# Kernel tuning notes

Measured on AMD Instinct MI355X. Metric: run time of the kernel, lower is better.

## Reference

```python
import jax, jax.numpy as jnp
import numpy as np

EMBED_DIM = 1024
NUM_HEADS = 16
HEAD_DIM = EMBED_DIM // NUM_HEADS


def setup_inputs() -> dict:
    key = jax.random.key(0)
    ks = jax.random.split(key, 9)
    B, T, C = 4, 2048, EMBED_DIM
    s = 1.0 / np.sqrt(C)
    return {
        "x": jax.random.normal(ks[0], (B, T, C), jnp.float32),
        "Wq": jax.random.normal(ks[1], (C, C), jnp.float32) * s,
        "bq": jnp.zeros((C,), jnp.float32),
        "Wk": jax.random.normal(ks[2], (C, C), jnp.float32) * s,
        "bk": jnp.zeros((C,), jnp.float32),
        "Wv": jax.random.normal(ks[3], (C, C), jnp.float32) * s,
        "bv": jnp.zeros((C,), jnp.float32),
        "Wo": jax.random.normal(ks[4], (C, C), jnp.float32) * s,
        "bo": jnp.zeros((C,), jnp.float32),
    }


def reference(x, Wq, bq, Wk, bk, Wv, bv, Wo, bo):
    B, T, C = x.shape
    H, D = NUM_HEADS, HEAD_DIM
    # projections (torch Linear: y = x @ W.T + b; here weights stored as [in, out])
    q = (x @ Wq + bq).reshape(B, T, H, D).transpose(0, 2, 1, 3)  # [B,H,T,D]
    k = (x @ Wk + bk).reshape(B, T, H, D).transpose(0, 2, 1, 3)
    v = (x @ Wv + bv).reshape(B, T, H, D).transpose(0, 2, 1, 3)
    scores = jnp.einsum("bhqd,bhkd->bhqk", q, k) / jnp.sqrt(jnp.float32(D))
    causal = jnp.tril(jnp.ones((T, T), bool))
    scores = jnp.where(causal, scores, -jnp.inf)
    attn = jax.nn.softmax(scores, axis=-1)
    out = jnp.einsum("bhqk,bhkd->bhqd", attn, v)  # [B,H,T,D]
    out = out.transpose(0, 2, 1, 3).reshape(B, T, C)
    return out @ Wo + bo
```

## Files before the change

### kernel.cpp

```cpp
#include <hip/hip_runtime.h>
#include <hip/hip_bf16.h>
#include <math.h>

typedef __hip_bfloat16 bf16_t;
typedef __attribute__((ext_vector_type(8))) short short8;
typedef __attribute__((ext_vector_type(4))) float floatx4;

#define T_SEQ 2048
#define NB    4
#define NH    16
#define HD    64
#define C_DIM 1024
#define M_ROWS (NB * T_SEQ)

#define Q_SCALE 0.18033688011f

__device__ __forceinline__ void load_lds16(const bf16_t* g, bf16_t* l) {
    __builtin_amdgcn_global_load_lds(
        (const __attribute__((address_space(1))) void*)g,
        (__attribute__((address_space(3))) void*)l,
        16, 0, 0);
}

__device__ __forceinline__ floatx4 mfma16(short8 a, short8 b, floatx4 c) {
    return __builtin_amdgcn_mfma_f32_16x16x32_bf16(a, b, c, 0, 0, 0);
}

__global__ void convert_x_kernel(const float* __restrict__ x, bf16_t* __restrict__ xb) {
    int i = blockIdx.x * 256 + threadIdx.x;
    float4 v = reinterpret_cast<const float4*>(x)[i];
    union { bf16_t h[4]; short4 s4; } u;
    u.h[0] = __float2bfloat16(v.x);
    u.h[1] = __float2bfloat16(v.y);
    u.h[2] = __float2bfloat16(v.z);
    u.h[3] = __float2bfloat16(v.w);
    reinterpret_cast<short4*>(xb)[i] = u.s4;
}

__global__ void transpose_cvt_kernel(const float* __restrict__ W0, const float* __restrict__ W1,
                                     const float* __restrict__ W2, const float* __restrict__ W3,
                                     bf16_t* __restrict__ O0, bf16_t* __restrict__ O1,
                                     bf16_t* __restrict__ O2, bf16_t* __restrict__ O3) {
    const float* W = (blockIdx.z == 0) ? W0 : (blockIdx.z == 1) ? W1 : (blockIdx.z == 2) ? W2 : W3;
    bf16_t*      O = (blockIdx.z == 0) ? O0 : (blockIdx.z == 1) ? O1 : (blockIdx.z == 2) ? O2 : O3;
    __shared__ float tile[32][33];
    int bx = blockIdx.x * 32, by = blockIdx.y * 32;
    int tx = threadIdx.x, ty = threadIdx.y;
#pragma unroll
    for (int j = 0; j < 32; j += 8)
        tile[ty + j][tx] = W[(size_t)(by + ty + j) * C_DIM + bx + tx];
    __syncthreads();
#pragma unroll
    for (int j = 0; j < 32; j += 8)
        O[(size_t)(bx + ty + j) * C_DIM + by + tx] = __float2bfloat16(tile[tx][ty + j]);
}

__device__ __forceinline__ void gemm_mainloop(const bf16_t* __restrict__ Ablk,
                                              const bf16_t* __restrict__ Bblk,
                                              bf16_t* As, bf16_t* Bs,
                                              floatx4 acc[4][4], int wave, int lane) {
    int lr = lane & 15, lq = lane >> 4;
    int wr = (wave >> 1) * 64, wc = (wave & 1) * 64;
    for (int kt = 0; kt < C_DIM; kt += 64) {
#pragma unroll
        for (int j = 0; j < 4; ++j) {
            int chunk = j * 256 + wave * 64 + lane;
            int r = chunk >> 3, ps = chunk & 7;
            int c = ((ps ^ (r & 7)) * 8);
            load_lds16(Ablk + (size_t)r * C_DIM + kt + c, As + chunk * 8);
            load_lds16(Bblk + (size_t)r * C_DIM + kt + c, Bs + chunk * 8);
        }
        __syncthreads();
#pragma unroll
        for (int kk = 0; kk < 2; ++kk) {
            short8 af[4], bfr[4];
            int psw = ((kk * 4 + lq) ^ (lr & 7)) * 8;
#pragma unroll
            for (int m = 0; m < 4; ++m)
                af[m] = *reinterpret_cast<const short8*>(As + (wr + m * 16 + lr) * 64 + psw);
#pragma unroll
            for (int n = 0; n < 4; ++n)
                bfr[n] = *reinterpret_cast<const short8*>(Bs + (wc + n * 16 + lr) * 64 + psw);
#pragma unroll
            for (int m = 0; m < 4; ++m)
#pragma unroll
                for (int n = 0; n < 4; ++n)
                    acc[m][n] = mfma16(af[m], bfr[n], acc[m][n]);
        }
        __syncthreads();
    }
}

__global__ __launch_bounds__(256, 3) void gemm_qkv_kernel(
    const bf16_t* __restrict__ xb,
    const bf16_t* __restrict__ WqT, const bf16_t* __restrict__ WkT, const bf16_t* __restrict__ WvT,
    const float* __restrict__ bq, const float* __restrict__ bk, const float* __restrict__ bv,
    bf16_t* __restrict__ Q, bf16_t* __restrict__ K, bf16_t* __restrict__ Vt) {
    __shared__ bf16_t As[128 * 64];
    __shared__ bf16_t Bs[128 * 64];
    int tid = threadIdx.x, wave = tid >> 6, lane = tid & 63;

    int f    = (int)blockIdx.x + ((int)blockIdx.y << 3) + ((int)blockIdx.z << 9);
    int xcd  = f & 7;
    int s    = f >> 3;
    int rloc = s & 7;
    int t2   = s >> 3;
    int colp = t2 & 7;
    int wsel = t2 >> 3;
    int row0 = (xcd * 8 + rloc) * 128;
    int col0 = colp * 128;

    const bf16_t* Wt  = (wsel == 0) ? WqT : (wsel == 1) ? WkT : WvT;
    const float* bias = (wsel == 0) ? bq : (wsel == 1) ? bk : bv;

    floatx4 acc[4][4] = {};
    gemm_mainloop(xb + (size_t)row0 * C_DIM, Wt + (size_t)col0 * C_DIM, As, Bs, acc, wave, lane);

    int lr = lane & 15, lq = lane >> 4;
    int wr = (wave >> 1) * 64, wc = (wave & 1) * 64;

    if (wsel == 2) {
#pragma unroll
        for (int nt = 0; nt < 4; ++nt) {
            int col = col0 + wc + nt * 16 + lr;
            float bvv = bias[col];
            int h = col >> 6, d = col & 63;
#pragma unroll
            for (int m = 0; m < 4; ++m) {
                int rowg0 = row0 + wr + m * 16 + lq * 4;
                int b = rowg0 >> 11, t0 = rowg0 & (T_SEQ - 1);
                union { bf16_t h4[4]; short4 s4; } u;
#pragma unroll
                for (int r = 0; r < 4; ++r)
                    u.h4[r] = __float2bfloat16(acc[m][nt][r] + bvv);
                *reinterpret_cast<short4*>(
                    &Vt[((size_t)((b * NH + h) * HD + d)) * T_SEQ + t0]) = u.s4;
            }
        }
    } else {
        float scale = (wsel == 0) ? Q_SCALE : 1.0f;
        bf16_t* outp = (wsel == 0) ? Q : K;
#pragma unroll
        for (int nt = 0; nt < 4; ++nt) {
            int col = col0 + wc + nt * 16 + lr;
            float bvv = bias[col];
            int h = col >> 6, d = col & 63;
#pragma unroll
            for (int m = 0; m < 4; ++m) {
#pragma unroll
                for (int r = 0; r < 4; ++r) {
                    int rowg = row0 + wr + m * 16 + lq * 4 + r;
                    int b = rowg >> 11, t = rowg & (T_SEQ - 1);
                    float val = (acc[m][nt][r] + bvv) * scale;
                    outp[((size_t)((b * NH + h) * T_SEQ + t)) * HD + d] =
                        __float2bfloat16(val);
                }
            }
        }
    }
}

__global__ __launch_bounds__(256, 3) void attn_kernel(
    const bf16_t* __restrict__ Q, const bf16_t* __restrict__ K,
    const bf16_t* __restrict__ Vt, bf16_t* __restrict__ ctx) {
    __shared__ __align__(16) bf16_t Ks[2][64 * 64];
    __shared__ __align__(16) bf16_t Vs[2][64 * 64];
    int tid = threadIdx.x, w = tid >> 6, lane = tid & 63;
    int lr = lane & 15, lq = lane >> 4;
    int xcd = (int)blockIdx.x;
    int y   = (int)blockIdx.y;
    int bh  = xcd * 8 + (y & 7);
    int qp  = y >> 3;
    int b = bh >> 4, h = bh & 15;

    const bf16_t* Kbase = K  + (size_t)bh * T_SEQ * HD;
    const bf16_t* Vbase = Vt + (size_t)bh * HD * T_SEQ;

#pragma unroll 1
    for (int pass = 0; pass < 2; ++pass) {
        int qt = pass ? qp : (15 - qp);
        int q0 = qt * 128;
        int ktiles = 2 * qt + 2;
        const bf16_t* Qbase = Q + ((size_t)bh * T_SEQ + q0) * HD;
        int buf = 0;

#pragma unroll
        for (int cc = 0; cc < 2; ++cc) {
            int ch = tid + cc * 256;
            int r = ch >> 3, ps = ch & 7;
            int c = (ps ^ (r & 7)) * 8;
            load_lds16(Kbase + (size_t)r * HD + c, Ks[0] + ch * 8);
            load_lds16(Vbase + (size_t)r * T_SEQ + c, Vs[0] + ch * 8);
        }

        short8 qf[2][2];
#pragma unroll
        for (int g = 0; g < 2; ++g)
#pragma unroll
            for (int kk = 0; kk < 2; ++kk)
                qf[g][kk] = *reinterpret_cast<const short8*>(
                    Qbase + (size_t)(w * 32 + g * 16 + lr) * HD + kk * 32 + lq * 8);

        floatx4 o[2][4] = {};
        float lpart[2] = {0.f, 0.f};

        for (int it = 0; it < ktiles; ++it) {
            int ktb = it * 64;
            __syncthreads();

            if (it + 1 < ktiles) {
                int nk0 = ktb + 64;
#pragma unroll
                for (int cc = 0; cc < 2; ++cc) {
                    int ch = tid + cc * 256;
                    int r = ch >> 3, ps = ch & 7;
                    int c = (ps ^ (r & 7)) * 8;
                    load_lds16(Kbase + (size_t)(nk0 + r) * HD + c, Ks[buf ^ 1] + ch * 8);
                    load_lds16(Vbase + (size_t)r * T_SEQ + nk0 + c, Vs[buf ^ 1] + ch * 8);
                }
            }

            const bf16_t* Kc = Ks[buf];
            const bf16_t* Vc = Vs[buf];
            bool maskit = (it >= ktiles - 2);

            short8 kf[4][2], vf[4][2];
#pragma unroll
            for (int kk = 0; kk < 2; ++kk) {
                int psw = ((kk * 4 + lq) ^ (lr & 7)) * 8;
#pragma unroll
                for (int n = 0; n < 4; ++n)
                    kf[n][kk] = *reinterpret_cast<const short8*>(
                        Kc + (n * 16 + lr) * 64 + psw);
            }
#pragma unroll
            for (int kk = 0; kk < 2; ++kk) {
                int psw = ((kk * 4 + lq) ^ (lr & 7)) * 8;
#pragma unroll
                for (int dt = 0; dt < 4; ++dt)
                    vf[dt][kk] = *reinterpret_cast<const short8*>(
                        Vc + (dt * 16 + lr) * 64 + psw);
            }

            short8 pf[2][2];
#pragma unroll
            for (int g = 0; g < 2; ++g) {
                floatx4 s[4] = {};
                __builtin_amdgcn_s_setprio(1);
#pragma unroll
                for (int kk = 0; kk < 2; ++kk)
#pragma unroll
                    for (int n = 0; n < 4; ++n)
                        s[n] = mfma16(kf[n][kk], qf[g][kk], s[n]);
                __builtin_amdgcn_s_setprio(0);

                if (maskit) {
                    int rowg = q0 + w * 32 + g * 16 + lr;
#pragma unroll
                    for (int n = 0; n < 4; ++n)
#pragma unroll
                        for (int r = 0; r < 4; ++r) {
                            int colg = ktb + n * 16 + lq * 4 + r;
                            if (colg > rowg) s[n][r] = -1e30f;
                        }
                }

#pragma unroll
                for (int n = 0; n < 4; ++n)
#pragma unroll
                    for (int r = 0; r < 4; ++r)
                        s[n][r] = __builtin_amdgcn_exp2f(s[n][r]);
                float p0 = (s[0][0] + s[0][1]) + (s[0][2] + s[0][3]);
                float p1 = (s[1][0] + s[1][1]) + (s[1][2] + s[1][3]);
                float p2 = (s[2][0] + s[2][1]) + (s[2][2] + s[2][3]);
                float p3 = (s[3][0] + s[3][1]) + (s[3][2] + s[3][3]);
                lpart[g] += (p0 + p1) + (p2 + p3);

                unsigned upk[4][2];
#pragma unroll
                for (int n = 0; n < 4; ++n) {
                    asm("v_cvt_pk_bf16_f32 %0, %1, %2"
                        : "=v"(upk[n][0]) : "v"(s[n][0]), "v"(s[n][1]));
                    asm("v_cvt_pk_bf16_f32 %0, %1, %2"
                        : "=v"(upk[n][1]) : "v"(s[n][2]), "v"(s[n][3]));
                }
#pragma unroll
                for (int kk = 0; kk < 2; ++kk) {
                    unsigned x0 = upk[2 * kk][0], y0 = upk[2 * kk + 1][0];
                    unsigned x1 = upk[2 * kk][1], y1 = upk[2 * kk + 1][1];
                    asm("v_permlane32_swap_b32 %0, %1" : "+v"(x0), "+v"(y0));
                    asm("v_permlane32_swap_b32 %0, %1" : "+v"(x1), "+v"(y1));
                    asm("v_permlane16_swap_b32 %0, %1" : "+v"(x0), "+v"(y0));
                    asm("v_permlane16_swap_b32 %0, %1" : "+v"(x1), "+v"(y1));
                    union { unsigned u4[4]; short8 s8; } pk;
                    pk.u4[0] = x0; pk.u4[1] = x1; pk.u4[2] = y0; pk.u4[3] = y1;
                    pf[g][kk] = pk.s8;
                }
            }

            __builtin_amdgcn_s_setprio(1);
#pragma unroll
            for (int g = 0; g < 2; ++g)
#pragma unroll
                for (int kk = 0; kk < 2; ++kk)
#pragma unroll
                    for (int dt = 0; dt < 4; ++dt)
                        o[g][dt] = mfma16(pf[g][kk], vf[dt][kk], o[g][dt]);
            __builtin_amdgcn_s_setprio(0);

            buf ^= 1;
        }

#pragma unroll
        for (int g = 0; g < 2; ++g) {
            float l = lpart[g];
            l += __shfl_xor(l, 16);
            l += __shfl_xor(l, 32);
            float inv = 1.0f / l;
#pragma unroll
            for (int r = 0; r < 4; ++r) {
                float invr = __shfl(inv, (lane & 48) | (lq * 4 + r));
                int t = q0 + w * 32 + g * 16 + lq * 4 + r;
#pragma unroll
                for (int dt = 0; dt < 4; ++dt) {
                    int d = dt * 16 + lr;
                    ctx[((size_t)(b * T_SEQ + t)) * C_DIM + h * HD + d] =
                        __float2bfloat16(o[g][dt][r] * invr);
                }
            }
        }
    }
}

__global__ __launch_bounds__(256, 3) void gemm_out_kernel(
    const bf16_t* __restrict__ Actx, const bf16_t* __restrict__ WoT,
    const float* __restrict__ bo, float* __restrict__ out) {
    __shared__ bf16_t As[128 * 64];
    __shared__ bf16_t Bs[128 * 64];
    int tid = threadIdx.x, wave = tid >> 6, lane = tid & 63;

    int f    = (int)blockIdx.x + ((int)blockIdx.y << 3);
    int xcd  = f & 7;
    int s    = f >> 3;
    int rloc = s & 7;
    int colp = s >> 3;
    int row0 = (xcd * 8 + rloc) * 128;
    int col0 = colp * 128;

    floatx4 acc[4][4] = {};
    gemm_mainloop(Actx + (size_t)row0 * C_DIM, WoT + (size_t)col0 * C_DIM, As, Bs, acc, wave, lane);
    int lr = lane & 15, lq = lane >> 4;
    int wr = (wave >> 1) * 64, wc = (wave & 1) * 64;
#pragma unroll
    for (int nt = 0; nt < 4; ++nt) {
        int col = col0 + wc + nt * 16 + lr;
        float bvv = bo[col];
#pragma unroll
        for (int m = 0; m < 4; ++m)
#pragma unroll
            for (int r = 0; r < 4; ++r) {
                int rowg = row0 + wr + m * 16 + lq * 4 + r;
                out[(size_t)rowg * C_DIM + col] = acc[m][nt][r] + bvv;
            }
    }
}

extern "C" void kernel_launch(void* const* d_in, const int* in_sizes, int n_in,
                              void* d_out, int out_size, void* d_ws, size_t ws_size,
                              hipStream_t stream) {
    const float* x  = (const float*)d_in[0];
    const float* Wq = (const float*)d_in[1];
    const float* bq = (const float*)d_in[2];
    const float* Wk = (const float*)d_in[3];
    const float* bk = (const float*)d_in[4];
    const float* Wv = (const float*)d_in[5];
    const float* bv = (const float*)d_in[6];
    const float* Wo = (const float*)d_in[7];
    const float* bo = (const float*)d_in[8];
    float* out = (float*)d_out;

    char* ws = (char*)d_ws;
    bf16_t* xb  = (bf16_t*)ws; ws += (size_t)M_ROWS * C_DIM * 2;
    bf16_t* WqT = (bf16_t*)ws; ws += (size_t)C_DIM * C_DIM * 2;
    bf16_t* WkT = (bf16_t*)ws; ws += (size_t)C_DIM * C_DIM * 2;
    bf16_t* WvT = (bf16_t*)ws; ws += (size_t)C_DIM * C_DIM * 2;
    bf16_t* WoT = (bf16_t*)ws; ws += (size_t)C_DIM * C_DIM * 2;
    bf16_t* Qb  = (bf16_t*)ws; ws += (size_t)M_ROWS * C_DIM * 2;
    bf16_t* Kb  = (bf16_t*)ws; ws += (size_t)M_ROWS * C_DIM * 2;
    bf16_t* Vtb = (bf16_t*)ws; ws += (size_t)M_ROWS * C_DIM * 2;
    bf16_t* ctx = (bf16_t*)ws; ws += (size_t)M_ROWS * C_DIM * 2;

    convert_x_kernel<<<(M_ROWS * C_DIM / 4) / 256, 256, 0, stream>>>(x, xb);
    transpose_cvt_kernel<<<dim3(32, 32, 4), dim3(32, 8), 0, stream>>>(
        Wq, Wk, Wv, Wo, WqT, WkT, WvT, WoT);
    gemm_qkv_kernel<<<dim3(8, 64, 3), 256, 0, stream>>>(
        xb, WqT, WkT, WvT, bq, bk, bv, Qb, Kb, Vtb);
    attn_kernel<<<dim3(8, 64), 256, 0, stream>>>(Qb, Kb, Vtb, ctx);
    gemm_out_kernel<<<dim3(8, 64), 256, 0, stream>>>(ctx, WoT, bo, out);
}
```

Baseline: 236.2 us.

## Merge conversion kernels and split attention into one query tile per block

The x-to-bf16 conversion and the weight transpose-convert are merged into a single launch, with the block id selecting the role, which saves one kernel launch. The attention kernel no longer pairs a long and a short causal q-tile inside one block. It launches twice as many blocks, each handling one q-tile, with launch bounds raised to 4 blocks per SIMD to allow higher occupancy. The aim is more parallelism and less serial work per block, at the cost of losing the explicit load balancing that the pairing gave and possible register pressure from the tighter bound.

```diff
diff --git a/kernel.cpp b/kernel.cpp
--- a/kernel.cpp
+++ b/kernel.cpp
@@ -26,26 +26,30 @@
     return __builtin_amdgcn_mfma_f32_16x16x32_bf16(a, b, c, 0, 0, 0);
 }
 
-__global__ void convert_x_kernel(const float* __restrict__ x, bf16_t* __restrict__ xb) {
-    int i = blockIdx.x * 256 + threadIdx.x;
-    float4 v = reinterpret_cast<const float4*>(x)[i];
-    union { bf16_t h[4]; short4 s4; } u;
-    u.h[0] = __float2bfloat16(v.x);
-    u.h[1] = __float2bfloat16(v.y);
-    u.h[2] = __float2bfloat16(v.z);
-    u.h[3] = __float2bfloat16(v.w);
-    reinterpret_cast<short4*>(xb)[i] = u.s4;
-}
-
-__global__ void transpose_cvt_kernel(const float* __restrict__ W0, const float* __restrict__ W1,
-                                     const float* __restrict__ W2, const float* __restrict__ W3,
-                                     bf16_t* __restrict__ O0, bf16_t* __restrict__ O1,
-                                     bf16_t* __restrict__ O2, bf16_t* __restrict__ O3) {
-    const float* W = (blockIdx.z == 0) ? W0 : (blockIdx.z == 1) ? W1 : (blockIdx.z == 2) ? W2 : W3;
-    bf16_t*      O = (blockIdx.z == 0) ? O0 : (blockIdx.z == 1) ? O1 : (blockIdx.z == 2) ? O2 : O3;
+__global__ void convert_all_kernel(const float* __restrict__ x, bf16_t* __restrict__ xb,
+                                   const float* __restrict__ W0, const float* __restrict__ W1,
+                                   const float* __restrict__ W2, const float* __restrict__ W3,
+                                   bf16_t* __restrict__ O0, bf16_t* __restrict__ O1,
+                                   bf16_t* __restrict__ O2, bf16_t* __restrict__ O3) {
     __shared__ float tile[32][33];
-    int bx = blockIdx.x * 32, by = blockIdx.y * 32;
-    int tx = threadIdx.x, ty = threadIdx.y;
+    int bid = (int)blockIdx.x;
+    if (bid < 8192) {
+        int i = bid * 256 + (int)threadIdx.x;
+        float4 v = reinterpret_cast<const float4*>(x)[i];
+        union { bf16_t h[4]; short4 s4; } u;
+        u.h[0] = __float2bfloat16(v.x);
+        u.h[1] = __float2bfloat16(v.y);
+        u.h[2] = __float2bfloat16(v.z);
+        u.h[3] = __float2bfloat16(v.w);
+        reinterpret_cast<short4*>(xb)[i] = u.s4;
+        return;
+    }
+    int zb = bid - 8192;
+    int z  = zb >> 10;
+    const float* W = (z == 0) ? W0 : (z == 1) ? W1 : (z == 2) ? W2 : W3;
+    bf16_t*      O = (z == 0) ? O0 : (z == 1) ? O1 : (z == 2) ? O2 : O3;
+    int bx = (zb & 31) * 32, by = ((zb >> 5) & 31) * 32;
+    int tx = (int)threadIdx.x & 31, ty = (int)threadIdx.x >> 5;
 #pragma unroll
     for (int j = 0; j < 32; j += 8)
         tile[ty + j][tx] = W[(size_t)(by + ty + j) * C_DIM + bx + tx];
@@ -160,7 +164,7 @@
     }
 }
 
-__global__ __launch_bounds__(256, 3) void attn_kernel(
+__global__ __launch_bounds__(256, 4) void attn_kernel(
     const bf16_t* __restrict__ Q, const bf16_t* __restrict__ K,
     const bf16_t* __restrict__ Vt, bf16_t* __restrict__ ctx) {
     __shared__ __align__(16) bf16_t Ks[2][64 * 64];
@@ -170,163 +174,158 @@
     int xcd = (int)blockIdx.x;
     int y   = (int)blockIdx.y;
     int bh  = xcd * 8 + (y & 7);
-    int qp  = y >> 3;
+    int qt  = 15 - (y >> 3);
     int b = bh >> 4, h = bh & 15;
 
     const bf16_t* Kbase = K  + (size_t)bh * T_SEQ * HD;
     const bf16_t* Vbase = Vt + (size_t)bh * HD * T_SEQ;
-
-#pragma unroll 1
-    for (int pass = 0; pass < 2; ++pass) {
-        int qt = pass ? qp : (15 - qp);
-        int q0 = qt * 128;
-        int ktiles = 2 * qt + 2;
-        const bf16_t* Qbase = Q + ((size_t)bh * T_SEQ + q0) * HD;
-        int buf = 0;
-
-#pragma unroll
-        for (int cc = 0; cc < 2; ++cc) {
-            int ch = tid + cc * 256;
-            int r = ch >> 3, ps = ch & 7;
-            int c = (ps ^ (r & 7)) * 8;
-            load_lds16(Kbase + (size_t)r * HD + c, Ks[0] + ch * 8);
-            load_lds16(Vbase + (size_t)r * T_SEQ + c, Vs[0] + ch * 8);
-        }
-
-        short8 qf[2][2];
+    int q0 = qt * 128;
+    int ktiles = 2 * qt + 2;
+    const bf16_t* Qbase = Q + ((size_t)bh * T_SEQ + q0) * HD;
+    int buf = 0;
+
+#pragma unroll
+    for (int cc = 0; cc < 2; ++cc) {
+        int ch = tid + cc * 256;
+        int r = ch >> 3, ps = ch & 7;
+        int c = (ps ^ (r & 7)) * 8;
+        load_lds16(Kbase + (size_t)r * HD + c, Ks[0] + ch * 8);
+        load_lds16(Vbase + (size_t)r * T_SEQ + c, Vs[0] + ch * 8);
+    }
+
+    short8 qf[2][2];
+#pragma unroll
+    for (int g = 0; g < 2; ++g)
+#pragma unroll
+        for (int kk = 0; kk < 2; ++kk)
+            qf[g][kk] = *reinterpret_cast<const short8*>(
+                Qbase + (size_t)(w * 32 + g * 16 + lr) * HD + kk * 32 + lq * 8);
+
+    floatx4 o[2][4] = {};
+    float lpart[2] = {0.f, 0.f};
+
+    for (int it = 0; it < ktiles; ++it) {
+        int ktb = it * 64;
+        __syncthreads();
+
+        if (it + 1 < ktiles) {
+            int nk0 = ktb + 64;
+#pragma unroll
+            for (int cc = 0; cc < 2; ++cc) {
+                int ch = tid + cc * 256;
+                int r = ch >> 3, ps = ch & 7;
+                int c = (ps ^ (r & 7)) * 8;
+                load_lds16(Kbase + (size_t)(nk0 + r) * HD + c, Ks[buf ^ 1] + ch * 8);
+                load_lds16(Vbase + (size_t)r * T_SEQ + nk0 + c, Vs[buf ^ 1] + ch * 8);
+            }
+        }
+
+        const bf16_t* Kc = Ks[buf];
+        const bf16_t* Vc = Vs[buf];
+        bool maskit = (it >= ktiles - 2);
+
+        short8 kf[4][2], vf[4][2];
+#pragma unroll
+        for (int kk = 0; kk < 2; ++kk) {
+            int psw = ((kk * 4 + lq) ^ (lr & 7)) * 8;
+#pragma unroll
+            for (int n = 0; n < 4; ++n)
+                kf[n][kk] = *reinterpret_cast<const short8*>(
+                    Kc + (n * 16 + lr) * 64 + psw);
+        }
+#pragma unroll
+        for (int kk = 0; kk < 2; ++kk) {
+            int psw = ((kk * 4 + lq) ^ (lr & 7)) * 8;
+#pragma unroll
+            for (int dt = 0; dt < 4; ++dt)
+                vf[dt][kk] = *reinterpret_cast<const short8*>(
+                    Vc + (dt * 16 + lr) * 64 + psw);
+        }
+
+        short8 pf[2][2];
+#pragma unroll
+        for (int g = 0; g < 2; ++g) {
+            floatx4 s[4] = {};
+            __builtin_amdgcn_s_setprio(1);
+#pragma unroll
+            for (int kk = 0; kk < 2; ++kk)
+#pragma unroll
+                for (int n = 0; n < 4; ++n)
+                    s[n] = mfma16(kf[n][kk], qf[g][kk], s[n]);
+            __builtin_amdgcn_s_setprio(0);
+
+            if (maskit) {
+                int rowg = q0 + w * 32 + g * 16 + lr;
+#pragma unroll
+                for (int n = 0; n < 4; ++n)
+#pragma unroll
+                    for (int r = 0; r < 4; ++r) {
+                        int colg = ktb + n * 16 + lq * 4 + r;
+                        if (colg > rowg) s[n][r] = -1e30f;
+                    }
+            }
+
+#pragma unroll
+            for (int n = 0; n < 4; ++n)
+#pragma unroll
+                for (int r = 0; r < 4; ++r)
+                    s[n][r] = __builtin_amdgcn_exp2f(s[n][r]);
+            float p0 = (s[0][0] + s[0][1]) + (s[0][2] + s[0][3]);
+            float p1 = (s[1][0] + s[1][1]) + (s[1][2] + s[1][3]);
+            float p2 = (s[2][0] + s[2][1]) + (s[2][2] + s[2][3]);
+            float p3 = (s[3][0] + s[3][1]) + (s[3][2] + s[3][3]);
+            lpart[g] += (p0 + p1) + (p2 + p3);
+
+            unsigned upk[4][2];
+#pragma unroll
+            for (int n = 0; n < 4; ++n) {
+                asm("v_cvt_pk_bf16_f32 %0, %1, %2"
+                    : "=v"(upk[n][0]) : "v"(s[n][0]), "v"(s[n][1]));
+                asm("v_cvt_pk_bf16_f32 %0, %1, %2"
+                    : "=v"(upk[n][1]) : "v"(s[n][2]), "v"(s[n][3]));
+            }
+#pragma unroll
+            for (int kk = 0; kk < 2; ++kk) {
+                unsigned x0 = upk[2 * kk][0], y0 = upk[2 * kk + 1][0];
+                unsigned x1 = upk[2 * kk][1], y1 = upk[2 * kk + 1][1];
+                asm("v_permlane32_swap_b32 %0, %1" : "+v"(x0), "+v"(y0));
+                asm("v_permlane32_swap_b32 %0, %1" : "+v"(x1), "+v"(y1));
+                asm("v_permlane16_swap_b32 %0, %1" : "+v"(x0), "+v"(y0));
+                asm("v_permlane16_swap_b32 %0, %1" : "+v"(x1), "+v"(y1));
+                union { unsigned u4[4]; short8 s8; } pk;
+                pk.u4[0] = x0; pk.u4[1] = x1; pk.u4[2] = y0; pk.u4[3] = y1;
+                pf[g][kk] = pk.s8;
+            }
+        }
+
+        __builtin_amdgcn_s_setprio(1);
 #pragma unroll
         for (int g = 0; g < 2; ++g)
 #pragma unroll
             for (int kk = 0; kk < 2; ++kk)
-                qf[g][kk] = *reinterpret_cast<const short8*>(
-                    Qbase + (size_t)(w * 32 + g * 16 + lr) * HD + kk * 32 + lq * 8);
-
-        floatx4 o[2][4] = {};
-        float lpart[2] = {0.f, 0.f};
-
-        for (int it = 0; it < ktiles; ++it) {
-            int ktb = it * 64;
-            __syncthreads();
-
-            if (it + 1 < ktiles) {
-                int nk0 = ktb + 64;
-#pragma unroll
-                for (int cc = 0; cc < 2; ++cc) {
-                    int ch = tid + cc * 256;
-                    int r = ch >> 3, ps = ch & 7;
-                    int c = (ps ^ (r & 7)) * 8;
-                    load_lds16(Kbase + (size_t)(nk0 + r) * HD + c, Ks[buf ^ 1] + ch * 8);
-                    load_lds16(Vbase + (size_t)r * T_SEQ + nk0 + c, Vs[buf ^ 1] + ch * 8);
-                }
-            }
-
-            const bf16_t* Kc = Ks[buf];
-            const bf16_t* Vc = Vs[buf];
-            bool maskit = (it >= ktiles - 2);
-
-            short8 kf[4][2], vf[4][2];
-#pragma unroll
-            for (int kk = 0; kk < 2; ++kk) {
-                int psw = ((kk * 4 + lq) ^ (lr & 7)) * 8;
-#pragma unroll
-                for (int n = 0; n < 4; ++n)
-                    kf[n][kk] = *reinterpret_cast<const short8*>(
-                        Kc + (n * 16 + lr) * 64 + psw);
-            }
-#pragma unroll
-            for (int kk = 0; kk < 2; ++kk) {
-                int psw = ((kk * 4 + lq) ^ (lr & 7)) * 8;
 #pragma unroll
                 for (int dt = 0; dt < 4; ++dt)
-                    vf[dt][kk] = *reinterpret_cast<const short8*>(
-                        Vc + (dt * 16 + lr) * 64 + psw);
-            }
-
-            short8 pf[2][2];
-#pragma unroll
-            for (int g = 0; g < 2; ++g) {
-                floatx4 s[4] = {};
-                __builtin_amdgcn_s_setprio(1);
-#pragma unroll
-                for (int kk = 0; kk < 2; ++kk)
-#pragma unroll
-                    for (int n = 0; n < 4; ++n)
-                        s[n] = mfma16(kf[n][kk], qf[g][kk], s[n]);
-                __builtin_amdgcn_s_setprio(0);
-
-                if (maskit) {
-                    int rowg = q0 + w * 32 + g * 16 + lr;
-#pragma unroll
-                    for (int n = 0; n < 4; ++n)
-#pragma unroll
-                        for (int r = 0; r < 4; ++r) {
-                            int colg = ktb + n * 16 + lq * 4 + r;
-                            if (colg > rowg) s[n][r] = -1e30f;
-                        }
-                }
-
-#pragma unroll
-                for (int n = 0; n < 4; ++n)
-#pragma unroll
-                    for (int r = 0; r < 4; ++r)
-                        s[n][r] = __builtin_amdgcn_exp2f(s[n][r]);
-                float p0 = (s[0][0] + s[0][1]) + (s[0][2] + s[0][3]);
-                float p1 = (s[1][0] + s[1][1]) + (s[1][2] + s[1][3]);
-                float p2 = (s[2][0] + s[2][1]) + (s[2][2] + s[2][3]);
-                float p3 = (s[3][0] + s[3][1]) + (s[3][2] + s[3][3]);
-                lpart[g] += (p0 + p1) + (p2 + p3);
-
-                unsigned upk[4][2];
-#pragma unroll
-                for (int n = 0; n < 4; ++n) {
-                    asm("v_cvt_pk_bf16_f32 %0, %1, %2"
-                        : "=v"(upk[n][0]) : "v"(s[n][0]), "v"(s[n][1]));
-                    asm("v_cvt_pk_bf16_f32 %0, %1, %2"
-                        : "=v"(upk[n][1]) : "v"(s[n][2]), "v"(s[n][3]));
-                }
-#pragma unroll
-                for (int kk = 0; kk < 2; ++kk) {
-                    unsigned x0 = upk[2 * kk][0], y0 = upk[2 * kk + 1][0];
-                    unsigned x1 = upk[2 * kk][1], y1 = upk[2 * kk + 1][1];
-                    asm("v_permlane32_swap_b32 %0, %1" : "+v"(x0), "+v"(y0));
-                    asm("v_permlane32_swap_b32 %0, %1" : "+v"(x1), "+v"(y1));
-                    asm("v_permlane16_swap_b32 %0, %1" : "+v"(x0), "+v"(y0));
-                    asm("v_permlane16_swap_b32 %0, %1" : "+v"(x1), "+v"(y1));
-                    union { unsigned u4[4]; short8 s8; } pk;
-                    pk.u4[0] = x0; pk.u4[1] = x1; pk.u4[2] = y0; pk.u4[3] = y1;
-                    pf[g][kk] = pk.s8;
-                }
-            }
-
-            __builtin_amdgcn_s_setprio(1);
-#pragma unroll
-            for (int g = 0; g < 2; ++g)
-#pragma unroll
-                for (int kk = 0; kk < 2; ++kk)
-#pragma unroll
-                    for (int dt = 0; dt < 4; ++dt)
-                        o[g][dt] = mfma16(pf[g][kk], vf[dt][kk], o[g][dt]);
-            __builtin_amdgcn_s_setprio(0);
-
-            buf ^= 1;
-        }
-
-#pragma unroll
-        for (int g = 0; g < 2; ++g) {
-            float l = lpart[g];
-            l += __shfl_xor(l, 16);
-            l += __shfl_xor(l, 32);
-            float inv = 1.0f / l;
-#pragma unroll
-            for (int r = 0; r < 4; ++r) {
-                float invr = __shfl(inv, (lane & 48) | (lq * 4 + r));
-                int t = q0 + w * 32 + g * 16 + lq * 4 + r;
-#pragma unroll
-                for (int dt = 0; dt < 4; ++dt) {
-                    int d = dt * 16 + lr;
-                    ctx[((size_t)(b * T_SEQ + t)) * C_DIM + h * HD + d] =
-                        __float2bfloat16(o[g][dt][r] * invr);
-                }
+                    o[g][dt] = mfma16(pf[g][kk], vf[dt][kk], o[g][dt]);
+        __builtin_amdgcn_s_setprio(0);
+
+        buf ^= 1;
+    }
+
+#pragma unroll
+    for (int g = 0; g < 2; ++g) {
+        float l = lpart[g];
+        l += __shfl_xor(l, 16);
+        l += __shfl_xor(l, 32);
+        float inv = 1.0f / l;
+#pragma unroll
+        for (int r = 0; r < 4; ++r) {
+            float invr = __shfl(inv, (lane & 48) | (lq * 4 + r));
+            int t = q0 + w * 32 + g * 16 + lq * 4 + r;
+#pragma unroll
+            for (int dt = 0; dt < 4; ++dt) {
+                int d = dt * 16 + lr;
+                ctx[((size_t)(b * T_SEQ + t)) * C_DIM + h * HD + d] =
+                    __float2bfloat16(o[g][dt][r] * invr);
             }
         }
     }
@@ -390,11 +389,10 @@
     bf16_t* Vtb = (bf16_t*)ws; ws += (size_t)M_ROWS * C_DIM * 2;
     bf16_t* ctx = (bf16_t*)ws; ws += (size_t)M_ROWS * C_DIM * 2;
 
-    convert_x_kernel<<<(M_ROWS * C_DIM / 4) / 256, 256, 0, stream>>>(x, xb);
-    transpose_cvt_kernel<<<dim3(32, 32, 4), dim3(32, 8), 0, stream>>>(
-        Wq, Wk, Wv, Wo, WqT, WkT, WvT, WoT);
+    convert_all_kernel<<<8192 + 4096, 256, 0, stream>>>(
+        x, xb, Wq, Wk, Wv, Wo, WqT, WkT, WvT, WoT);
     gemm_qkv_kernel<<<dim3(8, 64, 3), 256, 0, stream>>>(
         xb, WqT, WkT, WvT, bq, bk, bv, Qb, Kb, Vtb);
-    attn_kernel<<<dim3(8, 64), 256, 0, stream>>>(Qb, Kb, Vtb, ctx);
+    attn_kernel<<<dim3(8, 128), 256, 0, stream>>>(Qb, Kb, Vtb, ctx);
     gemm_out_kernel<<<dim3(8, 64), 256, 0, stream>>>(ctx, WoT, bo, out);
 }
```

After: 395.1 us. 67.3% more time.
